# Performance work log

Hardware: AMD Instinct MI355X
Metric: run time of the kernel (lower is better)

Reference implementation:

```python
import jax, jax.numpy as jnp
import numpy as np

N = 16384       # reservoir units (square)
B = 512         # flattened batch rows
NNZ = 131072    # non-zeros in sparse reservoir (avg degree 8)
R = 3           # recurrence_degree -> R+1 steps


def setup_inputs() -> dict:
    key = jax.random.key(0)
    k1, k2, k3, k4, k5, k6, k7 = jax.random.split(key, 7)
    x = jax.random.normal(k1, (B, N), dtype=jnp.float32)
    # sparse reservoir values, scaled for stable recurrence
    kernel = jax.random.normal(k2, (NNZ,), dtype=jnp.float32) * 0.05
    b_i = jax.random.normal(k3, (N,), dtype=jnp.float32) * 0.1
    b_f = jax.random.normal(k4, (N,), dtype=jnp.float32) * 0.1
    b_o = jax.random.normal(k5, (N,), dtype=jnp.float32) * 0.1
    b_g = jax.random.normal(k6, (N,), dtype=jnp.float32) * 0.1
    sparse_indices = jax.random.randint(k7, (NNZ, 2), 0, N, dtype=jnp.int64)
    return {"x": x, "kernel": kernel, "b_i": b_i, "b_f": b_f,
            "b_o": b_o, "b_g": b_g, "sparse_indices": sparse_indices}


def _spmm(h, rows, cols, vals):
    # y = h @ W_sparse, W in COO: y[:, c] += h[:, r] * v
    contrib = h.T[rows] * vals[:, None]              # (nnz, B)
    return jax.ops.segment_sum(contrib, cols, num_segments=N).T  # (B, N)


def reference(x, kernel, b_i, b_f, b_o, b_g, sparse_indices):
    rows = sparse_indices[:, 0]
    cols = sparse_indices[:, 1]
    h = x
    c = jnp.zeros_like(x)
    for _ in range(R + 1):
        z = _spmm(h, rows, cols, kernel)             # shared sparse reservoir matmul
        i = jax.nn.sigmoid(z + b_i)
        f = jax.nn.sigmoid(z + b_f)
        o = jax.nn.sigmoid(z + b_o)
        g = jnp.tanh(z + b_g)
        c = f * c + i * g
        h = o * jnp.tanh(c)
    return h
```

## Files before the change

kernel.cpp:

```cpp
#include <hip/hip_runtime.h>
#include <hip/hip_fp16.h>

#define N 16384
#define B 512
#define NNZ 131072
#define KMAX 16

__device__ __forceinline__ float rcp_(float x) {
    return __builtin_amdgcn_rcpf(x);
}
__device__ __forceinline__ float tanh_(float x) {
    return 1.f - 2.f * rcp_(__expf(2.f * x) + 1.f);
}
__device__ __forceinline__ __half2 as_h2(unsigned int u) {
    __half2 h;
    __builtin_memcpy(&h, &u, 4);
    return h;
}
__device__ __forceinline__ unsigned int pack_h2(float a, float b) {
    __half2 h = __halves2half2(__float2half_rn(a), __float2half_rn(b));
    unsigned int u;
    __builtin_memcpy(&u, &h, 4);
    return u;
}

__device__ __forceinline__ int is64_(const int* __restrict__ w) {
    int a = 1;
    #pragma unroll
    for (int i = 1; i < 16; i += 2) a &= (w[i] == 0);
    return a;
}

__global__ __launch_bounds__(256) void prep_kernel(
        const float* __restrict__ x, __half* __restrict__ xT,
        const int* __restrict__ w, const float* __restrict__ kern,
        int* __restrict__ counts, unsigned int* __restrict__ ell,
        uint2* __restrict__ ovf, int* __restrict__ ovf_cnt,
        const float* __restrict__ bi, const float* __restrict__ bf,
        const float* __restrict__ bo, const float* __restrict__ bg,
        float4* __restrict__ b4) {
    const int bid = blockIdx.x;
    const int t = threadIdx.x;
    if (bid < 8192) {
        __shared__ float tile[32][33];
        int bx = (bid & 511) * 32;
        int by = (bid >> 9) * 32;
        int tx = t & 31, ty = t >> 5;
        #pragma unroll
        for (int i = 0; i < 32; i += 8)
            tile[ty + i][tx] = x[(size_t)(by + ty + i) * N + bx + tx];
        __syncthreads();
        #pragma unroll
        for (int i = 0; i < 32; i += 8)
            xT[(size_t)(bx + ty + i) * B + by + tx] = __float2half(tile[tx][ty + i]);
    } else if (bid < 8704) {
        int k = (bid - 8192) * 256 + t;
        int is64 = is64_(w);
        int row = is64 ? w[4 * k]     : w[2 * k];
        int col = is64 ? w[4 * k + 2] : w[2 * k + 1];
        unsigned int packed = (unsigned int)(unsigned short)row |
                              ((unsigned int)__half_as_ushort(__float2half_rn(kern[k])) << 16);
        int slot = atomicAdd(&counts[col], 1);
        if (slot < KMAX) {
            ell[col * KMAX + slot] = packed;
        } else {
            int pos = atomicAdd(ovf_cnt, 1);
            ovf[pos] = make_uint2((unsigned int)col, packed);
        }
    } else {
        int i = (bid - 8704) * 256 + t;
        b4[i] = make_float4(__expf(-bi[i]), __expf(-bf[i]), __expf(-bo[i]),
                            __expf(-2.f * bg[i]));
    }
}

template <bool FIRST, bool LAST>
__global__ __launch_bounds__(256, 4) void lstm_iter_kernel(
        const uint4*  __restrict__ hin,
        uint4*        __restrict__ hout,
        uint4*        __restrict__ c,
        float*        __restrict__ out,
        const int*    __restrict__ counts,
        const uint4*  __restrict__ ell4,
        const uint2*  __restrict__ ovf,
        const int*    __restrict__ ovf_cnt,
        const float4* __restrict__ b4) {
    const int t      = threadIdx.x;
    const int lane16 = t & 15;
    const int sub    = t >> 4;
    const int q      = blockIdx.x & 3;
    const int col    = (blockIdx.x >> 2) * 16 + sub;
    const int boff   = q * 16 + lane16;

    uint4 e0 = ell4[col * 4 + 0];
    uint4 e1 = ell4[col * 4 + 1];
    uint4 e2 = ell4[col * 4 + 2];
    uint4 e3 = ell4[col * 4 + 3];
    unsigned int en[KMAX] = { e0.x, e0.y, e0.z, e0.w, e1.x, e1.y, e1.z, e1.w,
                              e2.x, e2.y, e2.z, e2.w, e3.x, e3.y, e3.z, e3.w };

    float z[8] = {0.f, 0.f, 0.f, 0.f, 0.f, 0.f, 0.f, 0.f};
    #pragma unroll
    for (int half = 0; half < 2; ++half) {
        uint4 hv[8];
        #pragma unroll
        for (int j = 0; j < 8; ++j)
            hv[j] = hin[(en[half * 8 + j] & 0xFFFFu) * (B / 8) + boff];
        #pragma unroll
        for (int j = 0; j < 8; ++j) {
            float v = __half2float(__ushort_as_half((unsigned short)(en[half * 8 + j] >> 16)));
            float2 f0 = __half22float2(as_h2(hv[j].x));
            float2 f1 = __half22float2(as_h2(hv[j].y));
            float2 f2 = __half22float2(as_h2(hv[j].z));
            float2 f3 = __half22float2(as_h2(hv[j].w));
            z[0] = fmaf(v, f0.x, z[0]);  z[1] = fmaf(v, f0.y, z[1]);
            z[2] = fmaf(v, f1.x, z[2]);  z[3] = fmaf(v, f1.y, z[3]);
            z[4] = fmaf(v, f2.x, z[4]);  z[5] = fmaf(v, f2.y, z[5]);
            z[6] = fmaf(v, f3.x, z[6]);  z[7] = fmaf(v, f3.y, z[7]);
        }
    }
    int cnt = counts[col];
    if (cnt > KMAX) {
        int novf = *ovf_cnt;
        for (int k = 0; k < novf; ++k) {
            uint2 o = ovf[k];
            if (o.x == (unsigned int)col) {
                unsigned int p = o.y;
                float v = __half2float(__ushort_as_half((unsigned short)(p >> 16)));
                uint4 hx = hin[(p & 0xFFFFu) * (B / 8) + boff];
                float2 f0 = __half22float2(as_h2(hx.x));
                float2 f1 = __half22float2(as_h2(hx.y));
                float2 f2 = __half22float2(as_h2(hx.z));
                float2 f3 = __half22float2(as_h2(hx.w));
                z[0] = fmaf(v, f0.x, z[0]);  z[1] = fmaf(v, f0.y, z[1]);
                z[2] = fmaf(v, f1.x, z[2]);  z[3] = fmaf(v, f1.y, z[3]);
                z[4] = fmaf(v, f2.x, z[4]);  z[5] = fmaf(v, f2.y, z[5]);
                z[6] = fmaf(v, f3.x, z[6]);  z[7] = fmaf(v, f3.y, z[7]);
            }
        }
    }

    const float4 bb = b4[col];
    const unsigned int idx = (unsigned int)col * (B / 8) + boff;

    float cv[8] = {0.f, 0.f, 0.f, 0.f, 0.f, 0.f, 0.f, 0.f};
    if (!FIRST) {
        uint4 cr = c[idx];
        float2 c0 = __half22float2(as_h2(cr.x));
        float2 c1 = __half22float2(as_h2(cr.y));
        float2 c2 = __half22float2(as_h2(cr.z));
        float2 c3 = __half22float2(as_h2(cr.w));
        cv[0] = c0.x; cv[1] = c0.y; cv[2] = c1.x; cv[3] = c1.y;
        cv[4] = c2.x; cv[5] = c2.y; cv[6] = c3.x; cv[7] = c3.y;
    }

    float hh[8], ch[8];
    #pragma unroll
    for (int e = 0; e < 8; ++e) {
        float ez = __expf(-z[e]);
        float ig = rcp_(fmaf(bb.x, ez, 1.f));
        float fg = rcp_(fmaf(bb.y, ez, 1.f));
        float og = rcp_(fmaf(bb.z, ez, 1.f));
        float dE = bb.w * ez * ez;
        float gg = fmaf(2.f, rcp_(1.f + dE), -1.f);
        float cn = fg * cv[e] + ig * gg;
        ch[e] = cn;
        hh[e] = og * tanh_(cn);
    }

    if (!LAST) {
        c[idx]    = make_uint4(pack_h2(ch[0], ch[1]), pack_h2(ch[2], ch[3]),
                               pack_h2(ch[4], ch[5]), pack_h2(ch[6], ch[7]));
        hout[idx] = make_uint4(pack_h2(hh[0], hh[1]), pack_h2(hh[2], hh[3]),
                               pack_h2(hh[4], hh[5]), pack_h2(hh[6], hh[7]));
    } else {
        __shared__ float tile[128 * 17];
        #pragma unroll
        for (int e = 0; e < 8; ++e)
            tile[(lane16 * 8 + e) * 17 + sub] = hh[e];
        __syncthreads();
        const int col0 = (blockIdx.x >> 2) * 16;
        #pragma unroll
        for (int k = 0; k < 8; ++k) {
            int i = k * 256 + t;
            int r = i >> 4;
            int cc = i & 15;
            out[(size_t)(q * 128 + r) * N + col0 + cc] = tile[r * 17 + cc];
        }
    }
}

extern "C" void kernel_launch(void* const* d_in, const int* in_sizes, int n_in,
                              void* d_out, int out_size, void* d_ws, size_t ws_size,
                              hipStream_t stream) {
    const float* x    = (const float*)d_in[0];
    const float* kern = (const float*)d_in[1];
    const float* b_i  = (const float*)d_in[2];
    const float* b_f  = (const float*)d_in[3];
    const float* b_o  = (const float*)d_in[4];
    const float* b_g  = (const float*)d_in[5];
    const int*   idxw = (const int*)d_in[6];

    char* ws = (char*)d_ws;
    uint4*        hA      = (uint4*)       (ws + 0);
    uint4*        hB      = (uint4*)       (ws + 16777216);
    uint4*        c       = (uint4*)       (ws + 33554432);
    unsigned int* ell     = (unsigned int*)(ws + 50331648);
    int*          counts  = (int*)         (ws + 51380224);
    int*          ovf_cnt = (int*)         (ws + 51445760);
    uint2*        ovf     = (uint2*)       (ws + 51445768);
    float4*       b4      = (float4*)      (ws + 51478656);

    hipMemsetAsync(ell, 0, 1048576 + 65536 + 4, stream);

    prep_kernel<<<8768, 256, 0, stream>>>(x, (__half*)hA, idxw, kern,
                                          counts, ell, ovf, ovf_cnt,
                                          b_i, b_f, b_o, b_g, b4);

    const uint4* ell4 = (const uint4*)ell;
    float* out = (float*)d_out;
    const int GRID = (N / 16) * 4;

    lstm_iter_kernel<true,  false><<<GRID, 256, 0, stream>>>(hA, hB, c, out, counts, ell4, ovf, ovf_cnt, b4);
    lstm_iter_kernel<false, false><<<GRID, 256, 0, stream>>>(hB, hA, c, out, counts, ell4, ovf, ovf_cnt, b4);
    lstm_iter_kernel<false, false><<<GRID, 256, 0, stream>>>(hA, hB, c, out, counts, ell4, ovf, ovf_cnt, b4);
    lstm_iter_kernel<false, true ><<<GRID, 256, 0, stream>>>(hB, hA, c, out, counts, ell4, ovf, ovf_cnt, b4);
}
```

Before: 208.8 us.

## Accumulate SpMM in packed half2 FMAs and remap blocks to 32 columns

The sparse gather-accumulate now uses packed fp16 FMAs (__hfma2) with half2 accumulators instead of converting every loaded value to fp32. The thread mapping also changes so each block covers 32 columns by 8 batch chunks rather than 16 by 16, with a matching output-transpose tile and grid size. The goal is to cut conversion ALU work and register use and to change gather coalescing per column. The cost is lower accumulation precision: fp16 sums can lose accuracy or overflow, and each contiguous gather segment shrinks from 256 to 128 bytes.

```diff
diff --git a/kernel.cpp b/kernel.cpp
--- a/kernel.cpp
+++ b/kernel.cpp
@@ -85,12 +85,12 @@
         const uint2*  __restrict__ ovf,
         const int*    __restrict__ ovf_cnt,
         const float4* __restrict__ b4) {
-    const int t      = threadIdx.x;
-    const int lane16 = t & 15;
-    const int sub    = t >> 4;
-    const int q      = blockIdx.x & 3;
-    const int col    = (blockIdx.x >> 2) * 16 + sub;
-    const int boff   = q * 16 + lane16;
+    const int t     = threadIdx.x;
+    const int lane8 = t & 7;
+    const int sub   = t >> 3;
+    const int q     = blockIdx.x & 7;
+    const int col   = (blockIdx.x >> 3) * 32 + sub;
+    const int boff  = q * 8 + lane8;
 
     uint4 e0 = ell4[col * 4 + 0];
     uint4 e1 = ell4[col * 4 + 1];
@@ -99,7 +99,7 @@
     unsigned int en[KMAX] = { e0.x, e0.y, e0.z, e0.w, e1.x, e1.y, e1.z, e1.w,
                               e2.x, e2.y, e2.z, e2.w, e3.x, e3.y, e3.z, e3.w };
 
-    float z[8] = {0.f, 0.f, 0.f, 0.f, 0.f, 0.f, 0.f, 0.f};
+    __half2 zp0 = __float2half2_rn(0.f), zp1 = zp0, zp2 = zp0, zp3 = zp0;
     #pragma unroll
     for (int half = 0; half < 2; ++half) {
         uint4 hv[8];
@@ -108,15 +108,12 @@
             hv[j] = hin[(en[half * 8 + j] & 0xFFFFu) * (B / 8) + boff];
         #pragma unroll
         for (int j = 0; j < 8; ++j) {
-            float v = __half2float(__ushort_as_half((unsigned short)(en[half * 8 + j] >> 16)));
-            float2 f0 = __half22float2(as_h2(hv[j].x));
-            float2 f1 = __half22float2(as_h2(hv[j].y));
-            float2 f2 = __half22float2(as_h2(hv[j].z));
-            float2 f3 = __half22float2(as_h2(hv[j].w));
-            z[0] = fmaf(v, f0.x, z[0]);  z[1] = fmaf(v, f0.y, z[1]);
-            z[2] = fmaf(v, f1.x, z[2]);  z[3] = fmaf(v, f1.y, z[3]);
-            z[4] = fmaf(v, f2.x, z[4]);  z[5] = fmaf(v, f2.y, z[5]);
-            z[6] = fmaf(v, f3.x, z[6]);  z[7] = fmaf(v, f3.y, z[7]);
+            __half  vh = __ushort_as_half((unsigned short)(en[half * 8 + j] >> 16));
+            __half2 vv = __half2half2(vh);
+            zp0 = __hfma2(vv, as_h2(hv[j].x), zp0);
+            zp1 = __hfma2(vv, as_h2(hv[j].y), zp1);
+            zp2 = __hfma2(vv, as_h2(hv[j].z), zp2);
+            zp3 = __hfma2(vv, as_h2(hv[j].w), zp3);
         }
     }
     int cnt = counts[col];
@@ -126,19 +123,22 @@
             uint2 o = ovf[k];
             if (o.x == (unsigned int)col) {
                 unsigned int p = o.y;
-                float v = __half2float(__ushort_as_half((unsigned short)(p >> 16)));
+                __half2 vv = __half2half2(__ushort_as_half((unsigned short)(p >> 16)));
                 uint4 hx = hin[(p & 0xFFFFu) * (B / 8) + boff];
-                float2 f0 = __half22float2(as_h2(hx.x));
-                float2 f1 = __half22float2(as_h2(hx.y));
-                float2 f2 = __half22float2(as_h2(hx.z));
-                float2 f3 = __half22float2(as_h2(hx.w));
-                z[0] = fmaf(v, f0.x, z[0]);  z[1] = fmaf(v, f0.y, z[1]);
-                z[2] = fmaf(v, f1.x, z[2]);  z[3] = fmaf(v, f1.y, z[3]);
-                z[4] = fmaf(v, f2.x, z[4]);  z[5] = fmaf(v, f2.y, z[5]);
-                z[6] = fmaf(v, f3.x, z[6]);  z[7] = fmaf(v, f3.y, z[7]);
+                zp0 = __hfma2(vv, as_h2(hx.x), zp0);
+                zp1 = __hfma2(vv, as_h2(hx.y), zp1);
+                zp2 = __hfma2(vv, as_h2(hx.z), zp2);
+                zp3 = __hfma2(vv, as_h2(hx.w), zp3);
             }
         }
     }
+
+    float z[8];
+    { float2 f;
+      f = __half22float2(zp0); z[0] = f.x; z[1] = f.y;
+      f = __half22float2(zp1); z[2] = f.x; z[3] = f.y;
+      f = __half22float2(zp2); z[4] = f.x; z[5] = f.y;
+      f = __half22float2(zp3); z[6] = f.x; z[7] = f.y; }
 
     const float4 bb = b4[col];
     const unsigned int idx = (unsigned int)col * (B / 8) + boff;
@@ -174,18 +174,18 @@
         hout[idx] = make_uint4(pack_h2(hh[0], hh[1]), pack_h2(hh[2], hh[3]),
                                pack_h2(hh[4], hh[5]), pack_h2(hh[6], hh[7]));
     } else {
-        __shared__ float tile[128 * 17];
+        __shared__ float tile[64 * 33];
         #pragma unroll
         for (int e = 0; e < 8; ++e)
-            tile[(lane16 * 8 + e) * 17 + sub] = hh[e];
+            tile[(lane8 * 8 + e) * 33 + sub] = hh[e];
         __syncthreads();
-        const int col0 = (blockIdx.x >> 2) * 16;
+        const int col0 = (blockIdx.x >> 3) * 32;
         #pragma unroll
         for (int k = 0; k < 8; ++k) {
             int i = k * 256 + t;
-            int r = i >> 4;
-            int cc = i & 15;
-            out[(size_t)(q * 128 + r) * N + col0 + cc] = tile[r * 17 + cc];
+            int r = i >> 5;
+            int cc = i & 31;
+            out[(size_t)(q * 64 + r) * N + col0 + cc] = tile[r * 33 + cc];
         }
     }
 }
@@ -219,7 +219,7 @@
 
     const uint4* ell4 = (const uint4*)ell;
     float* out = (float*)d_out;
-    const int GRID = (N / 16) * 4;
+    const int GRID = (N / 32) * 8;
 
     lstm_iter_kernel<true,  false><<<GRID, 256, 0, stream>>>(hA, hB, c, out, counts, ell4, ovf, ovf_cnt, b4);
     lstm_iter_kernel<false, false><<<GRID, 256, 0, stream>>>(hB, hA, c, out, counts, ell4, ovf, ovf_cnt, b4);
```

New measurement: 194.9 us. -6.6%, faster.
